# Performance work log

Hardware: AMD Instinct MI355X
Metric: run time of the kernel (lower is better)

Reference implementation:

```python
import jax, jax.numpy as jnp
import numpy as np

EPS = 1e-8

def squash(s, axis=-1):
    sq = jnp.sum(s * s, axis=axis, keepdims=True)
    return sq / (1.0 + sq) * s / (jnp.sqrt(sq) + EPS)

def setup_inputs() -> dict:
    key = jax.random.key(0)
    k1, k2 = jax.random.split(key)
    B, in_caps, in_dim = 256, 1152, 8
    num_caps, dim_caps = 10, 16
    x = jax.random.normal(k1, (B, in_caps, in_dim), dtype=jnp.float32)
    W = 0.01 * jax.random.normal(k2, (num_caps, in_caps, dim_caps, in_dim), dtype=jnp.float32)
    return {"x": x, "W": W}

def reference(x, W, num_routing=3):
    # u_hat: [B, num_caps, in_caps, dim_caps]
    u_hat = jnp.einsum('ncdi,bci->bncd', W, x)
    u_hat_det = jax.lax.stop_gradient(u_hat)
    B, N, C, D = u_hat.shape
    b = jnp.zeros((B, N, C, 1), dtype=u_hat.dtype)
    for _ in range(num_routing - 1):
        c = jax.nn.softmax(b, axis=1)                 # over num_caps
        s = jnp.sum(c * u_hat_det, axis=2)            # [B, N, D]
        v = squash(s)
        uv = jnp.einsum('bncd,bnd->bnc', u_hat_det, v)[..., None]
        b = b + uv
    c = jax.nn.softmax(b, axis=1)
    s = jnp.sum(c * u_hat, axis=2)
    v = squash(s)                                     # [B, N, D]
    return v
```

## Files before the change

kernel.cpp:

```cpp
#include <hip/hip_runtime.h>
#include <math.h>
#include <stdint.h>

#define B_N 256
#define C_N 1152
#define I_N 8
#define N_N 10
#define D_N 16

constexpr int C_PER    = 18;
constexpr int C_CHUNKS = C_N / C_PER;
constexpr int STAGE_C  = 6;
constexpr int N_STAGES = 3;
constexpr int BLOCK    = 256;

typedef short v8s __attribute__((ext_vector_type(8)));
typedef float v4f __attribute__((ext_vector_type(4)));

constexpr int POOL_BYTES = 34760;

constexpr size_t VSTG_FL = 16 * 16 * 164;
constexpr size_t PS_FL   = (size_t)C_CHUNKS * B_N * 160;
constexpr size_t WB_SH   = (size_t)C_N * 1280;
constexpr size_t XT_SH   = (size_t)1024 * 2304;

#define GLD16(g, l)                                                         \
    __builtin_amdgcn_global_load_lds(                                       \
        (const uint32_t __attribute__((address_space(1)))*)(g),             \
        (uint32_t __attribute__((address_space(3)))*)(l), 16, 0, 0)

__device__ __forceinline__ uint32_t bf16_rne(float f) {
    uint32_t u = __float_as_uint(f);
    return (u + 0x7FFFu + ((u >> 16) & 1u)) >> 16;
}
__device__ __forceinline__ uint32_t pack2(float a, float b) {
    return bf16_rne(a) | (bf16_rne(b) << 16);
}
__device__ __forceinline__ float bf2f(short s) {
    return __uint_as_float(((uint32_t)(uint16_t)s) << 16);
}

__global__ __launch_bounds__(BLOCK)
void conv_w(const float* __restrict__ W, short* __restrict__ Wb)
{
    const int c0 = blockIdx.x * 8;
    const int cc = threadIdx.x >> 5;
    const int k4 = threadIdx.x & 31;
    const float4* W4 = (const float4*)W;
    uint2* dst = (uint2*)Wb;
    for (int n = 0; n < N_N; ++n) {
        float4 v = W4[(size_t)n * 36864 + (size_t)(c0 + cc) * 32 + k4];
        dst[(((size_t)(c0 + cc) * 1280 + n * 128) >> 2) + k4] =
            make_uint2(pack2(v.x, v.y), pack2(v.z, v.w));
    }
}

__global__ __launch_bounds__(BLOCK)
void conv_x(const float* __restrict__ x, short* __restrict__ xt)
{
    const int tile  = blockIdx.x;
    const int chunk = tile >> 4;
    const int btile = tile & 15;
    const int c0    = chunk * C_PER;
    const int gb0   = btile * 16;
    const float4* x4 = (const float4*)x;
    uint2* dst = (uint2*)(xt + (size_t)tile * 2304);
    #pragma unroll
    for (int it = 0; it < 3; ++it) {
        int f = threadIdx.x + BLOCK * it;
        if (f < 576) {
            int b = f / 36, r = f - b * 36;
            float4 v = x4[(size_t)(gb0 + b) * 2304 + c0 * 2 + r];
            int cp = r >> 1, i0 = (r & 1) * 4;
            dst[((cp * 128 + b * 8 + i0) >> 2)] =
                make_uint2(pack2(v.x, v.y), pack2(v.z, v.w));
        }
    }
}

template <bool FIRST>
__global__ __launch_bounds__(BLOCK, 4)
void route_pass(const short* __restrict__ Wb, const short* __restrict__ xt,
                const float* __restrict__ vstG, float* __restrict__ p_s)
{
    __shared__ __align__(16) char pool[POOL_BYTES];
    short* Ws   = (short*)pool;
    short* xs   = (short*)(pool + 15360);
    float* vst  = (float*)(pool + 19968);
    float* cfl  = (float*)(pool + 30464);
    float* rz   = (float*)(pool + 34376);
    float* comb = (float*)pool;

    const int tid   = threadIdx.x;
    const int wv    = tid >> 6;
    const int lane  = tid & 63;
    const int b     = lane & 15;
    const int quad  = lane >> 4;
    const int chunk = blockIdx.x;
    const int btile = blockIdx.y;
    const int gb0   = btile * 16;
    const int c0    = chunk * C_PER;

    {
        const char* src = (const char*)(xt + (size_t)(chunk * 16 + btile) * 2304);
        #pragma unroll
        for (int it = 0; it < 2; ++it) {
            int f = tid + BLOCK * it;
            if (f < 288) GLD16(src + f * 16, (char*)xs + f * 16);
        }
    }
    if (!FIRST) {
        const char* src = (const char*)(vstG + (size_t)btile * 2624);
        #pragma unroll
        for (int it = 0; it < 3; ++it) {
            int f = tid + BLOCK * it;
            if (f < 656) GLD16(src + f * 16, (char*)vst + f * 16);
        }
    }

    const int ncnt = (wv < 2) ? 3 : 2;
    v4f sacc[3];
    sacc[0] = (v4f){0.f, 0.f, 0.f, 0.f};
    sacc[1] = (v4f){0.f, 0.f, 0.f, 0.f};
    sacc[2] = (v4f){0.f, 0.f, 0.f, 0.f};

    for (int st = 0; st < N_STAGES; ++st) {
        __syncthreads();
        {
            const char* src = (const char*)(Wb + (size_t)(c0 + st * STAGE_C) * 1280);
            #pragma unroll
            for (int it = 0; it < 4; ++it) {
                int f = tid + BLOCK * it;
                if (f < 960) GLD16(src + f * 16, (char*)Ws + f * 16);
            }
        }
        __syncthreads();

        if (!FIRST) {
            #pragma unroll
            for (int k = 0; k < 15; ++k) {
                const int idx = wv + 4 * k;
                const int c   = idx / 10;
                const int n   = idx - c * 10;
                v8s wa = {0, 0, 0, 0, 0, 0, 0, 0};
                if (quad == 0)
                    wa = *(const v8s*)(Ws + c * 1280 + n * 128 + b * 8);
                const v8s xb = *(const v8s*)(xs + (st * STAGE_C + c) * 128 + b * 8);
                v4f u = __builtin_amdgcn_mfma_f32_16x16x32_bf16(
                    wa, xb, (v4f){0.f, 0.f, 0.f, 0.f}, 0, 0, 0);
                const float4 v4 = *(const float4*)(vst + b * 164 + n * 16 + quad * 4);
                float l = u[0] * v4.x + u[1] * v4.y + u[2] * v4.z + u[3] * v4.w;
                l += __shfl_xor(l, 16);
                l += __shfl_xor(l, 32);
                const float e1 = __expf(l);
                if (quad == 0) cfl[c * 163 + n * 16 + b] = e1;
            }
            __syncthreads();
            if (tid < 96) {
                const int c = tid >> 4, bb = tid & 15;
                float Z = 0.f;
                #pragma unroll
                for (int n = 0; n < N_N; ++n) Z += cfl[c * 163 + n * 16 + bb];
                rz[c * 16 + bb] = __builtin_amdgcn_rcpf(Z);
            }
            __syncthreads();
        }

        #pragma unroll
        for (int Q = 0; Q < 2; ++Q) {
            const int  clq   = Q * 4 + quad;
            const bool valid = (clq < STAGE_C);
            const int  clql  = valid ? clq : 0;
            const v8s xq = *(const v8s*)(xs + (st * STAGE_C + clql) * 128 + b * 8);
            float xf[8];
            #pragma unroll
            for (int j = 0; j < 8; ++j) xf[j] = bf2f(xq[j]);
            #pragma unroll
            for (int jj = 0; jj < 3; ++jj) {
                if (jj < ncnt) {
                    const int n = wv + 4 * jj;
                    const float cv = FIRST ? 0.1f
                        : cfl[clql * 163 + n * 16 + b] * rz[clql * 16 + b];
                    union { v8s s; uint32_t u[4]; } zu;
                    zu.u[0] = pack2(cv * xf[0], cv * xf[1]);
                    zu.u[1] = pack2(cv * xf[2], cv * xf[3]);
                    zu.u[2] = pack2(cv * xf[4], cv * xf[5]);
                    zu.u[3] = pack2(cv * xf[6], cv * xf[7]);
                    v8s wa = {0, 0, 0, 0, 0, 0, 0, 0};
                    if (valid)
                        wa = *(const v8s*)(Ws + clql * 1280 + n * 128 + b * 8);
                    sacc[jj] = __builtin_amdgcn_mfma_f32_16x16x32_bf16(
                        wa, zu.s, sacc[jj], 0, 0, 0);
                }
            }
        }
    }

    __syncthreads();
    #pragma unroll
    for (int jj = 0; jj < 3; ++jj) {
        if (jj < ncnt) {
            const int n = wv + 4 * jj;
            #pragma unroll
            for (int r = 0; r < 4; ++r)
                comb[b * 164 + n * 16 + quad * 4 + r] = sacc[jj][r];
        }
    }
    __syncthreads();
    #pragma unroll
    for (int it = 0; it < 3; ++it) {
        int f = tid + BLOCK * it;
        if (f < 640) {
            int e = f * 4;
            int bb = e / 160, rem = e - bb * 160;
            float4 v = *(const float4*)(comb + bb * 164 + rem);
            *(float4*)(&p_s[((size_t)chunk * B_N + gb0 + bb) * 160 + rem]) = v;
        }
    }
}

__global__ __launch_bounds__(BLOCK)
void reduce_squash(const float* __restrict__ p_s, float* __restrict__ vstG,
                   float* __restrict__ out, int phase)
{
    const int warp = threadIdx.x >> 6;
    const int lane = threadIdx.x & 63;
    const int g    = blockIdx.x * 4 + warp;
    const int q    = lane & 3;
    const int h    = lane >> 2;

    float4 s = make_float4(0.f, 0.f, 0.f, 0.f);
    #pragma unroll
    for (int m = 0; m < C_CHUNKS / 16; ++m) {
        const int cc = h + 16 * m;
        float4 v = *(const float4*)(&p_s[((size_t)cc * (B_N * N_N) + g) * D_N + q * 4]);
        s.x += v.x; s.y += v.y; s.z += v.z; s.w += v.w;
    }
    #pragma unroll
    for (int off = 4; off < 64; off <<= 1) {
        s.x += __shfl_xor(s.x, off);
        s.y += __shfl_xor(s.y, off);
        s.z += __shfl_xor(s.z, off);
        s.w += __shfl_xor(s.w, off);
    }
    float sq = s.x * s.x + s.y * s.y + s.z * s.z + s.w * s.w;
    sq += __shfl_xor(sq, 1);
    sq += __shfl_xor(sq, 2);

    const float scale = (sq / (1.f + sq)) / (sqrtf(sq) + 1e-8f);
    const float4 v = make_float4(scale * s.x, scale * s.y, scale * s.z, scale * s.w);

    if (h == 0) {
        if (phase == 2) {
            *(float4*)(&out[(size_t)g * D_N + q * 4]) = v;
        } else {
            const int bb = g / 10, n = g - bb * 10;
            float* vp = vstG + (size_t)(bb >> 4) * 2624 + (bb & 15) * 164 + n * 16 + q * 4;
            if (phase == 0) {
                *(float4*)vp = v;
            } else {
                float4 o = *(const float4*)vp;
                *(float4*)vp = make_float4(o.x + v.x, o.y + v.y, o.z + v.z, o.w + v.w);
            }
        }
    }
}

extern "C" void kernel_launch(void* const* d_in, const int* in_sizes, int n_in,
                              void* d_out, int out_size, void* d_ws, size_t ws_size,
                              hipStream_t stream)
{
    const float* x = (const float*)d_in[0];
    const float* W = (const float*)d_in[1];
    float* out  = (float*)d_out;

    float* vstG = (float*)d_ws;
    float* p_s  = vstG + VSTG_FL;
    short* Wb   = (short*)(p_s + PS_FL);
    short* xt   = Wb + WB_SH;

    conv_w<<<dim3(C_N / 8), BLOCK, 0, stream>>>(W, Wb);
    conv_x<<<dim3(1024), BLOCK, 0, stream>>>(x, xt);

    dim3 grid(C_CHUNKS, 16);
    dim3 rgrid((B_N * N_N) / 4);

    route_pass<true><<<grid, BLOCK, 0, stream>>>(Wb, xt, vstG, p_s);
    reduce_squash<<<rgrid, BLOCK, 0, stream>>>(p_s, vstG, out, 0);
    route_pass<false><<<grid, BLOCK, 0, stream>>>(Wb, xt, vstG, p_s);
    reduce_squash<<<rgrid, BLOCK, 0, stream>>>(p_s, vstG, out, 1);
    route_pass<false><<<grid, BLOCK, 0, stream>>>(Wb, xt, vstG, p_s);
    reduce_squash<<<rgrid, BLOCK, 0, stream>>>(p_s, vstG, out, 2);
}
```

Baseline: 131.6 us.

## Double-buffer W stages, fuse conversion kernels, use hardware bf16 pack

Splits the W staging into six smaller stages held in a double-buffered LDS region, so the next stage's global-to-LDS loads are issued while the current stage computes. The softmax normaliser is now computed per lane, which removes a barrier and the shared rz array. The two precision-conversion kernels are merged into one launch, and the software round-to-nearest bf16 packing is replaced with the v_cvt_pk_bf16_f32 instruction. In exchange there are more stage iterations and barriers, and the manual waitcnt placement is fragile: a wrong count could read W data before it has landed.

```diff
diff --git a/kernel.cpp b/kernel.cpp
--- a/kernel.cpp
+++ b/kernel.cpp
@@ -10,14 +10,14 @@
 
 constexpr int C_PER    = 18;
 constexpr int C_CHUNKS = C_N / C_PER;
-constexpr int STAGE_C  = 6;
-constexpr int N_STAGES = 3;
+constexpr int STAGE_C  = 3;
+constexpr int N_STAGES = 6;
 constexpr int BLOCK    = 256;
 
 typedef short v8s __attribute__((ext_vector_type(8)));
 typedef float v4f __attribute__((ext_vector_type(4)));
 
-constexpr int POOL_BYTES = 34760;
+constexpr int POOL_BYTES = 32432;
 
 constexpr size_t VSTG_FL = 16 * 16 * 164;
 constexpr size_t PS_FL   = (size_t)C_CHUNKS * B_N * 160;
@@ -29,51 +29,48 @@
         (const uint32_t __attribute__((address_space(1)))*)(g),             \
         (uint32_t __attribute__((address_space(3)))*)(l), 16, 0, 0)
 
-__device__ __forceinline__ uint32_t bf16_rne(float f) {
-    uint32_t u = __float_as_uint(f);
-    return (u + 0x7FFFu + ((u >> 16) & 1u)) >> 16;
-}
-__device__ __forceinline__ uint32_t pack2(float a, float b) {
-    return bf16_rne(a) | (bf16_rne(b) << 16);
+__device__ __forceinline__ uint32_t cvtpk(float a, float b) {
+    uint32_t r;
+    asm("v_cvt_pk_bf16_f32 %0, %1, %2" : "=v"(r) : "v"(a), "v"(b));
+    return r;
 }
 __device__ __forceinline__ float bf2f(short s) {
     return __uint_as_float(((uint32_t)(uint16_t)s) << 16);
 }
 
 __global__ __launch_bounds__(BLOCK)
-void conv_w(const float* __restrict__ W, short* __restrict__ Wb)
+void conv_all(const float* __restrict__ x, const float* __restrict__ W,
+              short* __restrict__ Wb, short* __restrict__ xt)
 {
-    const int c0 = blockIdx.x * 8;
-    const int cc = threadIdx.x >> 5;
-    const int k4 = threadIdx.x & 31;
-    const float4* W4 = (const float4*)W;
-    uint2* dst = (uint2*)Wb;
-    for (int n = 0; n < N_N; ++n) {
-        float4 v = W4[(size_t)n * 36864 + (size_t)(c0 + cc) * 32 + k4];
-        dst[(((size_t)(c0 + cc) * 1280 + n * 128) >> 2) + k4] =
-            make_uint2(pack2(v.x, v.y), pack2(v.z, v.w));
-    }
-}
-
-__global__ __launch_bounds__(BLOCK)
-void conv_x(const float* __restrict__ x, short* __restrict__ xt)
-{
-    const int tile  = blockIdx.x;
-    const int chunk = tile >> 4;
-    const int btile = tile & 15;
-    const int c0    = chunk * C_PER;
-    const int gb0   = btile * 16;
-    const float4* x4 = (const float4*)x;
-    uint2* dst = (uint2*)(xt + (size_t)tile * 2304);
-    #pragma unroll
-    for (int it = 0; it < 3; ++it) {
-        int f = threadIdx.x + BLOCK * it;
-        if (f < 576) {
-            int b = f / 36, r = f - b * 36;
-            float4 v = x4[(size_t)(gb0 + b) * 2304 + c0 * 2 + r];
-            int cp = r >> 1, i0 = (r & 1) * 4;
-            dst[((cp * 128 + b * 8 + i0) >> 2)] =
-                make_uint2(pack2(v.x, v.y), pack2(v.z, v.w));
+    if (blockIdx.x < 144) {
+        const int c0 = blockIdx.x * 8;
+        const int cc = threadIdx.x >> 5;
+        const int k4 = threadIdx.x & 31;
+        const float4* W4 = (const float4*)W;
+        uint2* dst = (uint2*)Wb;
+        for (int n = 0; n < N_N; ++n) {
+            float4 v = W4[(size_t)n * 36864 + (size_t)(c0 + cc) * 32 + k4];
+            dst[(((size_t)(c0 + cc) * 1280 + n * 128) >> 2) + k4] =
+                make_uint2(cvtpk(v.x, v.y), cvtpk(v.z, v.w));
+        }
+    } else {
+        const int tile  = blockIdx.x - 144;
+        const int chunk = tile >> 4;
+        const int btile = tile & 15;
+        const int c0    = chunk * C_PER;
+        const int gb0   = btile * 16;
+        const float4* x4 = (const float4*)x;
+        uint2* dst = (uint2*)(xt + (size_t)tile * 2304);
+        #pragma unroll
+        for (int it = 0; it < 3; ++it) {
+            int f = threadIdx.x + BLOCK * it;
+            if (f < 576) {
+                int b = f / 36, r = f - b * 36;
+                float4 v = x4[(size_t)(gb0 + b) * 2304 + c0 * 2 + r];
+                int cp = r >> 1, i0 = (r & 1) * 4;
+                dst[((cp * 128 + b * 8 + i0) >> 2)] =
+                    make_uint2(cvtpk(v.x, v.y), cvtpk(v.z, v.w));
+            }
         }
     }
 }
@@ -84,11 +81,10 @@
                 const float* __restrict__ vstG, float* __restrict__ p_s)
 {
     __shared__ __align__(16) char pool[POOL_BYTES];
-    short* Ws   = (short*)pool;
+    short* wbuf = (short*)pool;
     short* xs   = (short*)(pool + 15360);
     float* vst  = (float*)(pool + 19968);
     float* cfl  = (float*)(pool + 30464);
-    float* rz   = (float*)(pool + 34376);
     float* comb = (float*)pool;
 
     const int tid   = threadIdx.x;
@@ -109,6 +105,7 @@
             if (f < 288) GLD16(src + f * 16, (char*)xs + f * 16);
         }
     }
+    asm volatile("" ::: "memory");
     if (!FIRST) {
         const char* src = (const char*)(vstG + (size_t)btile * 2624);
         #pragma unroll
@@ -117,6 +114,20 @@
             if (f < 656) GLD16(src + f * 16, (char*)vst + f * 16);
         }
     }
+    asm volatile("" ::: "memory");
+    #pragma unroll
+    for (int s0 = 0; s0 < 2; ++s0) {
+        const char* src = (const char*)(Wb + (size_t)(c0 + s0 * STAGE_C) * 1280);
+        char* dst = (char*)(wbuf + s0 * (STAGE_C * 1280));
+        #pragma unroll
+        for (int it = 0; it < 2; ++it) {
+            int f = tid + BLOCK * it;
+            if (f < 480) GLD16(src + f * 16, dst + f * 16);
+        }
+        asm volatile("" ::: "memory");
+    }
+    asm volatile("s_waitcnt vmcnt(2)" ::: "memory");
+    __builtin_amdgcn_s_barrier();
 
     const int ncnt = (wv < 2) ? 3 : 2;
     v4f sacc[3];
@@ -125,78 +136,102 @@
     sacc[2] = (v4f){0.f, 0.f, 0.f, 0.f};
 
     for (int st = 0; st < N_STAGES; ++st) {
-        __syncthreads();
-        {
-            const char* src = (const char*)(Wb + (size_t)(c0 + st * STAGE_C) * 1280);
+        const short* Ws = wbuf + (st & 1) * (STAGE_C * 1280);
+
+        if (st >= 1 && st < N_STAGES - 1) {
+            const char* src =
+                (const char*)(Wb + (size_t)(c0 + (st + 1) * STAGE_C) * 1280);
+            char* dst = (char*)(wbuf + ((st + 1) & 1) * (STAGE_C * 1280));
             #pragma unroll
-            for (int it = 0; it < 4; ++it) {
+            for (int it = 0; it < 2; ++it) {
                 int f = tid + BLOCK * it;
-                if (f < 960) GLD16(src + f * 16, (char*)Ws + f * 16);
-            }
-        }
-        __syncthreads();
+                if (f < 480) GLD16(src + f * 16, dst + f * 16);
+            }
+            asm volatile("" ::: "memory");
+        }
 
         if (!FIRST) {
             #pragma unroll
-            for (int k = 0; k < 15; ++k) {
+            for (int k = 0; k < 8; ++k) {
                 const int idx = wv + 4 * k;
-                const int c   = idx / 10;
-                const int n   = idx - c * 10;
-                v8s wa = {0, 0, 0, 0, 0, 0, 0, 0};
-                if (quad == 0)
-                    wa = *(const v8s*)(Ws + c * 1280 + n * 128 + b * 8);
-                const v8s xb = *(const v8s*)(xs + (st * STAGE_C + c) * 128 + b * 8);
-                v4f u = __builtin_amdgcn_mfma_f32_16x16x32_bf16(
-                    wa, xb, (v4f){0.f, 0.f, 0.f, 0.f}, 0, 0, 0);
-                const float4 v4 = *(const float4*)(vst + b * 164 + n * 16 + quad * 4);
-                float l = u[0] * v4.x + u[1] * v4.y + u[2] * v4.z + u[3] * v4.w;
-                l += __shfl_xor(l, 16);
-                l += __shfl_xor(l, 32);
-                const float e1 = __expf(l);
-                if (quad == 0) cfl[c * 163 + n * 16 + b] = e1;
-            }
-            __syncthreads();
-            if (tid < 96) {
-                const int c = tid >> 4, bb = tid & 15;
-                float Z = 0.f;
-                #pragma unroll
-                for (int n = 0; n < N_N; ++n) Z += cfl[c * 163 + n * 16 + bb];
-                rz[c * 16 + bb] = __builtin_amdgcn_rcpf(Z);
-            }
-            __syncthreads();
-        }
-
-        #pragma unroll
-        for (int Q = 0; Q < 2; ++Q) {
-            const int  clq   = Q * 4 + quad;
-            const bool valid = (clq < STAGE_C);
-            const int  clql  = valid ? clq : 0;
-            const v8s xq = *(const v8s*)(xs + (st * STAGE_C + clql) * 128 + b * 8);
+                if (idx < 30) {
+                    const int c = idx / 10;
+                    const int n = idx - c * 10;
+                    v8s wa = {0, 0, 0, 0, 0, 0, 0, 0};
+                    if (quad == 0)
+                        wa = *(const v8s*)(Ws + c * 1280 + n * 128 + b * 8);
+                    const v8s xb =
+                        *(const v8s*)(xs + (st * STAGE_C + c) * 128 + b * 8);
+                    v4f u = __builtin_amdgcn_mfma_f32_16x16x32_bf16(
+                        wa, xb, (v4f){0.f, 0.f, 0.f, 0.f}, 0, 0, 0);
+                    const float4 v4 =
+                        *(const float4*)(vst + b * 164 + n * 16 + quad * 4);
+                    float l = u[0] * v4.x + u[1] * v4.y + u[2] * v4.z + u[3] * v4.w;
+                    l += __shfl_xor(l, 16);
+                    l += __shfl_xor(l, 32);
+                    const float e1 = __expf(l);
+                    if (quad == 0) cfl[c * 163 + n * 16 + b] = e1;
+                }
+            }
+            asm volatile("s_waitcnt lgkmcnt(0)" ::: "memory");
+            __builtin_amdgcn_s_barrier();
+        }
+
+        {
+            const bool valid = (quad < STAGE_C);
+            const int  cl    = valid ? quad : 0;
+            const v8s xq =
+                *(const v8s*)(xs + (st * STAGE_C + cl) * 128 + b * 8);
             float xf[8];
             #pragma unroll
             for (int j = 0; j < 8; ++j) xf[j] = bf2f(xq[j]);
-            #pragma unroll
-            for (int jj = 0; jj < 3; ++jj) {
-                if (jj < ncnt) {
-                    const int n = wv + 4 * jj;
-                    const float cv = FIRST ? 0.1f
-                        : cfl[clql * 163 + n * 16 + b] * rz[clql * 16 + b];
-                    union { v8s s; uint32_t u[4]; } zu;
-                    zu.u[0] = pack2(cv * xf[0], cv * xf[1]);
-                    zu.u[1] = pack2(cv * xf[2], cv * xf[3]);
-                    zu.u[2] = pack2(cv * xf[4], cv * xf[5]);
-                    zu.u[3] = pack2(cv * xf[6], cv * xf[7]);
-                    v8s wa = {0, 0, 0, 0, 0, 0, 0, 0};
-                    if (valid)
-                        wa = *(const v8s*)(Ws + clql * 1280 + n * 128 + b * 8);
-                    sacc[jj] = __builtin_amdgcn_mfma_f32_16x16x32_bf16(
-                        wa, zu.s, sacc[jj], 0, 0, 0);
+
+            if (FIRST) {
+                union { v8s s; uint32_t u[4]; } zu;
+                zu.u[0] = cvtpk(0.1f * xf[0], 0.1f * xf[1]);
+                zu.u[1] = cvtpk(0.1f * xf[2], 0.1f * xf[3]);
+                zu.u[2] = cvtpk(0.1f * xf[4], 0.1f * xf[5]);
+                zu.u[3] = cvtpk(0.1f * xf[6], 0.1f * xf[7]);
+                #pragma unroll
+                for (int jj = 0; jj < 3; ++jj) {
+                    if (jj < ncnt) {
+                        const int n = wv + 4 * jj;
+                        v8s wa = {0, 0, 0, 0, 0, 0, 0, 0};
+                        if (valid)
+                            wa = *(const v8s*)(Ws + cl * 1280 + n * 128 + b * 8);
+                        sacc[jj] = __builtin_amdgcn_mfma_f32_16x16x32_bf16(
+                            wa, zu.s, sacc[jj], 0, 0, 0);
+                    }
                 }
-            }
-        }
-    }
-
-    __syncthreads();
+            } else {
+                float Z = 0.f;
+                #pragma unroll
+                for (int n = 0; n < N_N; ++n) Z += cfl[cl * 163 + n * 16 + b];
+                const float rzv = __builtin_amdgcn_rcpf(Z);
+                #pragma unroll
+                for (int jj = 0; jj < 3; ++jj) {
+                    if (jj < ncnt) {
+                        const int n = wv + 4 * jj;
+                        const float cv = cfl[cl * 163 + n * 16 + b] * rzv;
+                        union { v8s s; uint32_t u[4]; } zu;
+                        zu.u[0] = cvtpk(cv * xf[0], cv * xf[1]);
+                        zu.u[1] = cvtpk(cv * xf[2], cv * xf[3]);
+                        zu.u[2] = cvtpk(cv * xf[4], cv * xf[5]);
+                        zu.u[3] = cvtpk(cv * xf[6], cv * xf[7]);
+                        v8s wa = {0, 0, 0, 0, 0, 0, 0, 0};
+                        if (valid)
+                            wa = *(const v8s*)(Ws + cl * 1280 + n * 128 + b * 8);
+                        sacc[jj] = __builtin_amdgcn_mfma_f32_16x16x32_bf16(
+                            wa, zu.s, sacc[jj], 0, 0, 0);
+                    }
+                }
+            }
+        }
+
+        asm volatile("s_waitcnt vmcnt(0) lgkmcnt(0)" ::: "memory");
+        __builtin_amdgcn_s_barrier();
+    }
+
     #pragma unroll
     for (int jj = 0; jj < 3; ++jj) {
         if (jj < ncnt) {
@@ -279,8 +314,7 @@
     short* Wb   = (short*)(p_s + PS_FL);
     short* xt   = Wb + WB_SH;
 
-    conv_w<<<dim3(C_N / 8), BLOCK, 0, stream>>>(W, Wb);
-    conv_x<<<dim3(1024), BLOCK, 0, stream>>>(x, xt);
+    conv_all<<<dim3(144 + 1024), BLOCK, 0, stream>>>(x, W, Wb, xt);
 
     dim3 grid(C_CHUNKS, 16);
     dim3 rgrid((B_N * N_N) / 4);
```

New measurement: 129.7 us. Within noise of the previous version (-1.4%).
